# Optimization experiments

Hardware: AMD Instinct MI355X
Metric: run time of the kernel (lower is better)

## Reference

```python
import jax, jax.numpy as jnp
import numpy as np

NUM_RELATION = 7

def setup_inputs() -> dict:
    key = jax.random.key(0)
    ks = jax.random.split(key, 12)
    N, E, D, DO, R, DE = 20000, 640000, 512, 512, NUM_RELATION, 59
    inp = {
        "node_feat": jax.random.normal(ks[0], (N, D), dtype=jnp.float32),
        "edge_weight": jax.random.uniform(ks[1], (E,), dtype=jnp.float32),
        "edge_feat": jax.random.normal(ks[2], (E, DE), dtype=jnp.float32),
        "W_lin": jax.random.normal(ks[3], (DO, R * D), dtype=jnp.float32) * 0.02,
        "b_lin": jax.random.normal(ks[4], (DO,), dtype=jnp.float32) * 0.02,
        "W_self": jax.random.normal(ks[5], (DO, D), dtype=jnp.float32) * 0.02,
        "b_self": jax.random.normal(ks[6], (DO,), dtype=jnp.float32) * 0.02,
        "W_edge": jax.random.normal(ks[7], (DO, DE), dtype=jnp.float32) * 0.02,
        "b_edge": jax.random.normal(ks[8], (DO,), dtype=jnp.float32) * 0.02,
        "node_in": jax.random.randint(ks[9], (E,), 0, N, dtype=jnp.int64) if jax.config.jax_enable_x64 else jax.random.randint(ks[9], (E,), 0, N).astype(jnp.int32),
        "node_out": jax.random.randint(ks[10], (E,), 0, N).astype(jnp.int32),
        "relation": jax.random.randint(ks[11], (E,), 0, R).astype(jnp.int32),
    }
    inp["node_in"] = inp["node_in"].astype(jnp.int32)
    return inp


def reference(node_feat, edge_weight, edge_feat, W_lin, b_lin, W_self, b_self,
              W_edge, b_edge, node_in, node_out, relation):
    N, D = node_feat.shape
    R = NUM_RELATION
    # segment id: node_out * R + relation  (column index in sparse (N, N*R) adjacency)
    seg = node_out * R + relation  # [E]
    # update = adjacency.T @ input  == scatter-add of weighted source features
    msg = node_feat[node_in] * edge_weight[:, None]               # [E, D]
    update = jax.ops.segment_sum(msg, seg, num_segments=N * R)    # [N*R, D]
    # edge_linear path: edge_update scattered with the same segment ids
    edge_msg = (edge_feat @ W_edge.T + b_edge) * edge_weight[:, None]  # [E, D]
    update = update + jax.ops.segment_sum(edge_msg, seg, num_segments=N * R)
    update = update.reshape(N, R * D)                             # [N, R*D]
    # combine: linear(update) + self_loop(input), then relu
    out = update @ W_lin.T + b_lin + node_feat @ W_self.T + b_self
    return jax.nn.relu(out)
```

## Files before the change

kernel.cpp:

```cpp
#include <hip/hip_runtime.h>
#include <stdint.h>

typedef unsigned short u16;
typedef __attribute__((ext_vector_type(8))) __bf16 bf16x8;
typedef __attribute__((ext_vector_type(8))) unsigned short u16x8;
typedef __attribute__((ext_vector_type(4))) float f32x4;

#define NREL 7
#define DIM  512
#define DEDGE 59
#define KC   420
#define KCP  448
#define KU   3584
#define KTOT 4544

__device__ __forceinline__ float bf2f(u16 u) {
  union { unsigned u; float f; } c; c.u = ((unsigned)u) << 16; return c.f;
}
__device__ __forceinline__ u16 f2bf(float f) {
  union { float f; unsigned u; } c; c.f = f;
  unsigned r = ((c.u >> 16) & 1u) + 0x7FFFu;
  return (u16)((c.u + r) >> 16);
}

__device__ __forceinline__ void gload16(const void* g, void* l) {
  __builtin_amdgcn_global_load_lds(
      (__attribute__((address_space(1))) void*)g,
      (__attribute__((address_space(3))) void*)l, 16, 0, 0);
}

__global__ void convA(const float* __restrict__ in, u16* __restrict__ out, int total4) {
  int i = blockIdx.x * 256 + threadIdx.x;
  if (i >= total4) return;
  float4 v = ((const float4*)in)[i];
  ushort4 r;
  r.x = f2bf(v.x); r.y = f2bf(v.y); r.z = f2bf(v.z); r.w = f2bf(v.w);
  ((ushort4*)out)[i] = r;
}

__global__ void buildBW(const float* __restrict__ W_lin, const float* __restrict__ W_self,
                        u16* __restrict__ Bfull, int total4) {
  int gid = blockIdx.x * 256 + threadIdx.x;
  if (gid >= total4) return;
  int idx = gid * 4;
  int o = idx >> 12;
  int k = idx & 4095;
  const float* src = (k < KU) ? (W_lin + (size_t)o * KU + k)
                              : (W_self + (size_t)o * DIM + (k - KU));
  float4 v = *(const float4*)src;
  ushort4 rr;
  rr.x = f2bf(v.x); rr.y = f2bf(v.y); rr.z = f2bf(v.z); rr.w = f2bf(v.w);
  *(ushort4*)(Bfull + (size_t)o * KTOT + k) = rr;
}

__global__ __launch_bounds__(512) void buildCx(const float* __restrict__ W_edge,
                                               const float* __restrict__ b_edge,
                                               const float* __restrict__ W_lin,
                                               u16* __restrict__ Bfull) {
  int c = blockIdx.x;
  int o = threadIdx.x;
  u16* dst = Bfull + (size_t)o * KTOT + KU + DIM;
  if (c >= KC) { dst[c] = 0; return; }
  __shared__ float col[DIM];
  int r;
  if (c < NREL * DEDGE) {
    r = c / DEDGE;
    int de = c - r * DEDGE;
    col[o] = W_edge[(size_t)o * DEDGE + de];
  } else {
    r = c - NREL * DEDGE;
    col[o] = b_edge[o];
  }
  __syncthreads();
  const float* wrow = W_lin + (size_t)o * KU + (size_t)r * DIM;
  float acc = 0.f;
#pragma unroll 8
  for (int d = 0; d < DIM; ++d) acc += col[d] * wrow[d];
  dst[c] = f2bf(acc);
}

__global__ void countK2(const int* __restrict__ node_out, const int* __restrict__ relation,
                        int* __restrict__ counts2, int E) {
  int e = blockIdx.x * 256 + threadIdx.x;
  if (e < E) atomicAdd(&counts2[node_out[e] * 8 + relation[e]], 1);
}

__global__ void baseK(const int* __restrict__ counts2, int* __restrict__ offs2,
                      int* __restrict__ cursor2, int* __restrict__ totalCtr, int N) {
  int n = blockIdx.x * 256 + threadIdx.x;
  if (n >= N) return;
  int cnt[NREL];
  int s = 0;
#pragma unroll
  for (int r = 0; r < NREL; ++r) { cnt[r] = counts2[n * 8 + r]; s += cnt[r]; }
  int base = atomicAdd(totalCtr, s);
#pragma unroll
  for (int r = 0; r < NREL; ++r) {
    offs2[n * 8 + r] = base;
    cursor2[n * 8 + r] = base;
    base += cnt[r];
  }
  offs2[n * 8 + 7] = base;
}

__global__ void fillK2(const int* __restrict__ node_in, const int* __restrict__ node_out,
                       const int* __restrict__ relation, const float* __restrict__ ew,
                       int* __restrict__ cursor2, uint4* __restrict__ quads, int E) {
  int e = blockIdx.x * 256 + threadIdx.x;
  if (e >= E) return;
  int p = atomicAdd(&cursor2[node_out[e] * 8 + relation[e]], 1);
  quads[p] = make_uint4((unsigned)node_in[e], __float_as_uint(ew[e]), (unsigned)e, 0u);
}

__global__ __launch_bounds__(256) void aggK(const u16* __restrict__ NF,
                                            const float* __restrict__ ef,
                                            const uint4* __restrict__ quads,
                                            const int* __restrict__ offs2,
                                            u16* __restrict__ U,
                                            u16* __restrict__ G) {
  int n = blockIdx.x;
  int wid = threadIdx.x >> 6, lane = threadIdx.x & 63;
  int o0 = lane * 8;
  u16* urow = U + (size_t)n * KU;
  u16* grow = G + (size_t)n * KCP;
  if (wid == 3 && lane < KCP - KC) grow[KC + lane] = 0;
  int base = n * 8;
  for (int r = wid; r < NREL; r += 4) {
    int p0 = offs2[base + r], p1 = offs2[base + r + 1];
    float a[8];
#pragma unroll
    for (int j = 0; j < 8; ++j) a[j] = 0.f;
    float ag = 0.f;
    if (p0 < p1) {
      uint4 q = quads[p0];
      for (int p = p0; p < p1; ++p) {
        uint4 qn = (p + 1 < p1) ? quads[p + 1] : q;
        int src = __builtin_amdgcn_readfirstlane((int)q.x);
        float w = __uint_as_float(__builtin_amdgcn_readfirstlane(q.y));
        int e = __builtin_amdgcn_readfirstlane((int)q.z);
        u16x8 hv = *(const u16x8*)(NF + (size_t)src * DIM + o0);
        float vef = (lane < DEDGE) ? ef[(size_t)e * DEDGE + lane] : 1.0f;
#pragma unroll
        for (int j = 0; j < 8; ++j) a[j] += w * bf2f(hv[j]);
        ag += w * vef;
        q = qn;
      }
    }
    u16x8 st;
#pragma unroll
    for (int j = 0; j < 8; ++j) st[j] = f2bf(a[j]);
    *(u16x8*)(urow + (size_t)r * DIM + o0) = st;
    if (lane < DEDGE) grow[r * DEDGE + lane] = f2bf(ag);
    else if (lane == DEDGE) grow[NREL * DEDGE + r] = f2bf(ag);
  }
}

__global__ __launch_bounds__(256) void gemm_br(const u16* __restrict__ U,
                                               const u16* __restrict__ NF,
                                               const u16* __restrict__ G,
                                               const u16* __restrict__ Bt,
                                               const float* __restrict__ b_lin,
                                               const float* __restrict__ b_self,
                                               float* __restrict__ Cout, int M) {
  __shared__ __align__(16) u16 sA[3][128 * 32];
  __shared__ __align__(16) u16 sB[3][128 * 32];
  const int tid = threadIdx.x;
  const int w = tid >> 6, l = tid & 63;
  const int lr = l & 15, kg = l >> 4;
  const int sl = kg ^ ((lr >> 1) & 3);

  const int id = blockIdx.x;
  const int npan = gridDim.x >> 2;
  const int nfull = (npan >> 3) << 3;
  int p, c;
  if (id < nfull * 4) {
    int g = id >> 5, r = id & 31;
    p = g * 8 + (r & 7);
    c = r >> 3;
  } else {
    int t = id - nfull * 4;
    p = nfull + (t >> 2);
    c = t & 3;
  }
  const int m0 = p * 128, n0 = c * 128;
  const int wr = w >> 1, wc = w & 1;
  f32x4 acc[4][4];
  const f32x4 z4 = {0.f, 0.f, 0.f, 0.f};
#pragma unroll
  for (int i = 0; i < 4; ++i)
#pragma unroll
    for (int j = 0; j < 4; ++j) acc[i][j] = z4;

  const int ktiles = KTOT / 32;

  auto stage = [&](int kt, int b) {
    const u16* Ab; int astr, ac0;
    if (kt < 112)      { Ab = U;  astr = KU;  ac0 = kt * 32; }
    else if (kt < 128) { Ab = NF; astr = DIM; ac0 = kt * 32 - KU; }
    else               { Ab = G;  astr = KCP; ac0 = kt * 32 - (KU + DIM); }
    const int k0 = kt * 32;
#pragma unroll
    for (int t = 0; t < 2; ++t) {
      int idx = w * 128 + t * 64 + l;
      int row = idx >> 2, kp = idx & 3;
      int s = kp ^ ((row >> 1) & 3);
      int gm = m0 + row; gm = gm < M ? gm : M - 1;
      gload16(Ab + (size_t)gm * astr + ac0 + s * 8,
              (char*)sA[b] + (size_t)idx * 16);
    }
#pragma unroll
    for (int t = 0; t < 2; ++t) {
      int idx = w * 128 + t * 64 + l;
      int row = idx >> 2, kp = idx & 3;
      int s = kp ^ ((row >> 1) & 3);
      gload16(Bt + (size_t)(n0 + row) * KTOT + k0 + s * 8,
              (char*)sB[b] + (size_t)idx * 16);
    }
  };

  stage(0, 0);
  stage(1, 1);
  asm volatile("s_waitcnt vmcnt(4)" ::: "memory");
  __builtin_amdgcn_s_barrier();
  __builtin_amdgcn_sched_barrier(0);

  for (int kt = 0; kt < ktiles; ++kt) {
    const int cur = kt % 3;
    if (kt + 2 < ktiles) stage(kt + 2, (kt + 2) % 3);
    bf16x8 af[4], bfr[4];
#pragma unroll
    for (int i = 0; i < 4; ++i)
      af[i] = *(const bf16x8*)(sA[cur] + (size_t)(wr * 64 + i * 16 + lr) * 32 + sl * 8);
#pragma unroll
    for (int j = 0; j < 4; ++j)
      bfr[j] = *(const bf16x8*)(sB[cur] + (size_t)(wc * 64 + j * 16 + lr) * 32 + sl * 8);
#pragma unroll
    for (int i = 0; i < 4; ++i)
#pragma unroll
      for (int j = 0; j < 4; ++j)
        acc[i][j] = __builtin_amdgcn_mfma_f32_16x16x32_bf16(af[i], bfr[j], acc[i][j], 0, 0, 0);
    if (kt + 2 < ktiles) {
      asm volatile("s_waitcnt vmcnt(4)" ::: "memory");
    } else {
      asm volatile("s_waitcnt vmcnt(0)" ::: "memory");
    }
    __builtin_amdgcn_s_barrier();
    __builtin_amdgcn_sched_barrier(0);
  }
#pragma unroll
  for (int i = 0; i < 4; ++i) {
#pragma unroll
    for (int j = 0; j < 4; ++j) {
      int gj = n0 + wc * 64 + j * 16 + lr;
      float bias = b_lin[gj] + b_self[gj];
#pragma unroll
      for (int v = 0; v < 4; ++v) {
        int gm = m0 + wr * 64 + i * 16 + kg * 4 + v;
        if (gm < M)
          ((float*)Cout)[(size_t)gm * DIM + gj] = fmaxf(acc[i][j][v] + bias, 0.f);
      }
    }
  }
}

extern "C" void kernel_launch(void* const* d_in, const int* in_sizes, int n_in,
                              void* d_out, int out_size, void* d_ws, size_t ws_size,
                              hipStream_t stream) {
  const float* node_feat = (const float*)d_in[0];
  const float* edge_weight = (const float*)d_in[1];
  const float* edge_feat = (const float*)d_in[2];
  const float* W_lin = (const float*)d_in[3];
  const float* b_lin = (const float*)d_in[4];
  const float* W_self = (const float*)d_in[5];
  const float* b_self = (const float*)d_in[6];
  const float* W_edge = (const float*)d_in[7];
  const float* b_edge = (const float*)d_in[8];
  const int* node_in = (const int*)d_in[9];
  const int* node_out = (const int*)d_in[10];
  const int* relation = (const int*)d_in[11];
  float* out = (float*)d_out;

  const int N = in_sizes[0] / DIM;
  const int E = in_sizes[1];

  char* ws = (char*)d_ws;
  size_t off = 0;
  auto take = [&](size_t b) {
    char* p = ws + off;
    off += (b + 255) & ~(size_t)255;
    return p;
  };
  u16* NF       = (u16*)take((size_t)N * DIM * 2);
  u16* Bfull    = (u16*)take((size_t)DIM * KTOT * 2);
  u16* U        = (u16*)take((size_t)N * KU * 2);
  u16* G        = (u16*)take((size_t)N * KCP * 2);
  int* counts2  = (int*)take((size_t)N * 8 * 4);
  int* offs2    = (int*)take((size_t)N * 8 * 4);
  int* cursor2  = (int*)take((size_t)N * 8 * 4);
  int* totalCtr = (int*)take(256);
  uint4* quads  = (uint4*)take((size_t)E * 16);
  if (off > ws_size) return;

  hipMemsetAsync(counts2, 0, (size_t)N * 8 * 4, stream);
  hipMemsetAsync(totalCtr, 0, 256, stream);

  {
    int total4 = N * DIM / 4;
    convA<<<(total4 + 255) / 256, 256, 0, stream>>>(node_feat, NF, total4);
  }
  {
    int total4 = DIM * 4096 / 4;
    buildBW<<<(total4 + 255) / 256, 256, 0, stream>>>(W_lin, W_self, Bfull, total4);
  }
  buildCx<<<KCP, 512, 0, stream>>>(W_edge, b_edge, W_lin, Bfull);

  countK2<<<(E + 255) / 256, 256, 0, stream>>>(node_out, relation, counts2, E);
  baseK<<<(N + 255) / 256, 256, 0, stream>>>(counts2, offs2, cursor2, totalCtr, N);
  fillK2<<<(E + 255) / 256, 256, 0, stream>>>(node_in, node_out, relation, edge_weight,
                                              cursor2, quads, E);

  aggK<<<N, 256, 0, stream>>>(NF, edge_feat, quads, offs2, U, G);

  {
    int npan = (N + 127) / 128;
    gemm_br<<<npan * 4, 256, 0, stream>>>(U, NF, G, Bfull, b_lin, b_self, out, N);
  }
}
```

Measured before the change: 547.7 us.

## Split aggregation into edge-feature gather and column-partitioned node-feature gather

The single fused aggregation kernel is split into two launches. One handles the edge-feature weighted sums per node. The other uses 8 blocks of 64 threads per node, each covering a 64-column slice. Within a block, 8 edge groups process edges in parallel and are then reduced with cross-lane shuffles. This aims to expose more memory-level parallelism on the irregular gather, instead of one wave walking every edge of a relation serially. The cost is more blocks, repeated reads of the quad list per column slice, and a second launch.

```diff
diff --git a/kernel.cpp b/kernel.cpp
--- a/kernel.cpp
+++ b/kernel.cpp
@@ -112,46 +112,69 @@
   quads[p] = make_uint4((unsigned)node_in[e], __float_as_uint(ew[e]), (unsigned)e, 0u);
 }
 
-__global__ __launch_bounds__(256) void aggK(const u16* __restrict__ NF,
-                                            const float* __restrict__ ef,
-                                            const uint4* __restrict__ quads,
-                                            const int* __restrict__ offs2,
-                                            u16* __restrict__ U,
-                                            u16* __restrict__ G) {
-  int n = blockIdx.x;
-  int wid = threadIdx.x >> 6, lane = threadIdx.x & 63;
-  int o0 = lane * 8;
+__global__ __launch_bounds__(64) void aggP(const u16* __restrict__ NF,
+                                           const uint4* __restrict__ quads,
+                                           const int* __restrict__ offs2,
+                                           u16* __restrict__ U, int N) {
+  int bid = blockIdx.x;
+  int dp = bid / N;
+  int n  = bid - dp * N;
+  int l = threadIdx.x;
+  int grp = l >> 3, gl = l & 7;
+  int c0 = dp * 64 + gl * 8;
+  int base = n * 8;
   u16* urow = U + (size_t)n * KU;
-  u16* grow = G + (size_t)n * KCP;
-  if (wid == 3 && lane < KCP - KC) grow[KC + lane] = 0;
-  int base = n * 8;
-  for (int r = wid; r < NREL; r += 4) {
+  for (int r = 0; r < NREL; ++r) {
     int p0 = offs2[base + r], p1 = offs2[base + r + 1];
     float a[8];
 #pragma unroll
     for (int j = 0; j < 8; ++j) a[j] = 0.f;
-    float ag = 0.f;
-    if (p0 < p1) {
-      uint4 q = quads[p0];
-      for (int p = p0; p < p1; ++p) {
-        uint4 qn = (p + 1 < p1) ? quads[p + 1] : q;
-        int src = __builtin_amdgcn_readfirstlane((int)q.x);
-        float w = __uint_as_float(__builtin_amdgcn_readfirstlane(q.y));
-        int e = __builtin_amdgcn_readfirstlane((int)q.z);
-        u16x8 hv = *(const u16x8*)(NF + (size_t)src * DIM + o0);
-        float vef = (lane < DEDGE) ? ef[(size_t)e * DEDGE + lane] : 1.0f;
-#pragma unroll
-        for (int j = 0; j < 8; ++j) a[j] += w * bf2f(hv[j]);
-        ag += w * vef;
-        q = qn;
-      }
-    }
-    u16x8 st;
-#pragma unroll
-    for (int j = 0; j < 8; ++j) st[j] = f2bf(a[j]);
-    *(u16x8*)(urow + (size_t)r * DIM + o0) = st;
-    if (lane < DEDGE) grow[r * DEDGE + lane] = f2bf(ag);
-    else if (lane == DEDGE) grow[NREL * DEDGE + r] = f2bf(ag);
+    for (int p = p0 + grp; p < p1; p += 8) {
+      uint4 q = quads[p];
+      float w = __uint_as_float(q.y);
+      int src = (int)q.x;
+      u16x8 hv = *(const u16x8*)(NF + (size_t)src * DIM + c0);
+#pragma unroll
+      for (int j = 0; j < 8; ++j) a[j] += w * bf2f(hv[j]);
+    }
+#pragma unroll
+    for (int j = 0; j < 8; ++j) {
+      a[j] += __shfl_xor(a[j], 8);
+      a[j] += __shfl_xor(a[j], 16);
+      a[j] += __shfl_xor(a[j], 32);
+    }
+    if (grp == 0) {
+      u16x8 st;
+#pragma unroll
+      for (int j = 0; j < 8; ++j) st[j] = f2bf(a[j]);
+      *(u16x8*)(urow + (size_t)r * DIM + c0) = st;
+    }
+  }
+}
+
+__global__ __launch_bounds__(64) void gatherG2(const float* __restrict__ ef,
+                                               const uint4* __restrict__ quads,
+                                               const int* __restrict__ offs2,
+                                               u16* __restrict__ G) {
+  int n = blockIdx.x;
+  int lane = threadIdx.x;
+  u16* grow = G + (size_t)n * KCP;
+  int base = n * 8;
+  for (int r = 0; r < NREL; ++r) {
+    int p0 = offs2[base + r], p1 = offs2[base + r + 1];
+    float acc = 0.f;
+    for (int p = p0; p < p1; ++p) {
+      uint4 q = quads[p];
+      int e = __builtin_amdgcn_readfirstlane((int)q.z);
+      float w = __uint_as_float(__builtin_amdgcn_readfirstlane(q.y));
+      float v = (lane < DEDGE) ? ef[(size_t)e * DEDGE + lane] : 1.0f;
+      acc += w * v;
+    }
+    if (lane < DEDGE) grow[r * DEDGE + lane] = f2bf(acc);
+    else if (lane == DEDGE) grow[NREL * DEDGE + r] = f2bf(acc);
+  }
+  if (lane >= 60) {
+    for (int c = KC + (lane - 60); c < KCP; c += 4) grow[c] = 0;
   }
 }
 
@@ -319,7 +342,8 @@
   fillK2<<<(E + 255) / 256, 256, 0, stream>>>(node_in, node_out, relation, edge_weight,
                                               cursor2, quads, E);
 
-  aggK<<<N, 256, 0, stream>>>(NF, edge_feat, quads, offs2, U, G);
+  gatherG2<<<N, 64, 0, stream>>>(edge_feat, quads, offs2, G);
+  aggP<<<8 * N, 64, 0, stream>>>(NF, quads, offs2, U, N);
 
   {
     int npan = (N + 127) / 128;
```

Measured after the change: 643.4 us. +17.5%, slower.

## Split edge-feature and node-feature aggregation into separate block roles; vectorize buildCx

Applied to the files above, without the earlier changes.

The aggregation kernel now launches two kinds of blocks. One kind has each wavefront handle a single node and accumulate the edge-feature sums across all relations. The other kind only gathers node features per relation, so the gather loop no longer also reads edge features. This is meant to cut per-iteration latency and balance the work better. In exchange it drops the quad prefetch and reads the quad list twice. buildCx also switches to float4 loads of W_lin.

```diff
diff --git a/kernel.cpp b/kernel.cpp
--- a/kernel.cpp
+++ b/kernel.cpp
@@ -72,10 +72,14 @@
     col[o] = b_edge[o];
   }
   __syncthreads();
-  const float* wrow = W_lin + (size_t)o * KU + (size_t)r * DIM;
+  const float4* wv = (const float4*)(W_lin + (size_t)o * KU + (size_t)r * DIM);
   float acc = 0.f;
-#pragma unroll 8
-  for (int d = 0; d < DIM; ++d) acc += col[d] * wrow[d];
+#pragma unroll 4
+  for (int d4 = 0; d4 < DIM / 4; ++d4) {
+    float4 wq = wv[d4];
+    acc += col[d4 * 4 + 0] * wq.x + col[d4 * 4 + 1] * wq.y
+         + col[d4 * 4 + 2] * wq.z + col[d4 * 4 + 3] * wq.w;
+  }
   dst[c] = f2bf(acc);
 }
 
@@ -112,46 +116,59 @@
   quads[p] = make_uint4((unsigned)node_in[e], __float_as_uint(ew[e]), (unsigned)e, 0u);
 }
 
-__global__ __launch_bounds__(256) void aggK(const u16* __restrict__ NF,
-                                            const float* __restrict__ ef,
-                                            const uint4* __restrict__ quads,
-                                            const int* __restrict__ offs2,
-                                            u16* __restrict__ U,
-                                            u16* __restrict__ G) {
-  int n = blockIdx.x;
+__global__ __launch_bounds__(256) void aggBoth(const u16* __restrict__ NF,
+                                               const float* __restrict__ ef,
+                                               const uint4* __restrict__ quads,
+                                               const int* __restrict__ offs2,
+                                               u16* __restrict__ U,
+                                               u16* __restrict__ G,
+                                               int N, int ngg) {
+  int bid = blockIdx.x;
   int wid = threadIdx.x >> 6, lane = threadIdx.x & 63;
-  int o0 = lane * 8;
-  u16* urow = U + (size_t)n * KU;
-  u16* grow = G + (size_t)n * KCP;
-  if (wid == 3 && lane < KCP - KC) grow[KC + lane] = 0;
-  int base = n * 8;
-  for (int r = wid; r < NREL; r += 4) {
-    int p0 = offs2[base + r], p1 = offs2[base + r + 1];
-    float a[8];
-#pragma unroll
-    for (int j = 0; j < 8; ++j) a[j] = 0.f;
-    float ag = 0.f;
-    if (p0 < p1) {
-      uint4 q = quads[p0];
+  if (bid < ngg) {
+    int n = bid * 4 + wid;
+    if (n >= N) return;
+    u16* grow = G + (size_t)n * KCP;
+    int base = n * 8;
+    for (int r = 0; r < NREL; ++r) {
+      int p0 = offs2[base + r], p1 = offs2[base + r + 1];
+      float acc = 0.f;
       for (int p = p0; p < p1; ++p) {
-        uint4 qn = (p + 1 < p1) ? quads[p + 1] : q;
+        uint4 q = quads[p];
+        int e = __builtin_amdgcn_readfirstlane((int)q.z);
+        float w = __uint_as_float(__builtin_amdgcn_readfirstlane(q.y));
+        float v = (lane < DEDGE) ? ef[(size_t)e * DEDGE + lane] : 1.0f;
+        acc += w * v;
+      }
+      if (lane < DEDGE) grow[r * DEDGE + lane] = f2bf(acc);
+      else if (lane == DEDGE) grow[NREL * DEDGE + r] = f2bf(acc);
+    }
+    if (lane >= 60) {
+      for (int c = KC + (lane - 60); c < KCP; c += 4) grow[c] = 0;
+    }
+  } else {
+    int n = bid - ngg;
+    int o0 = lane * 8;
+    u16* urow = U + (size_t)n * KU;
+    int base = n * 8;
+    for (int r = wid; r < NREL; r += 4) {
+      int p0 = offs2[base + r], p1 = offs2[base + r + 1];
+      float a[8];
+#pragma unroll
+      for (int j = 0; j < 8; ++j) a[j] = 0.f;
+      for (int p = p0; p < p1; ++p) {
+        uint4 q = quads[p];
         int src = __builtin_amdgcn_readfirstlane((int)q.x);
         float w = __uint_as_float(__builtin_amdgcn_readfirstlane(q.y));
-        int e = __builtin_amdgcn_readfirstlane((int)q.z);
         u16x8 hv = *(const u16x8*)(NF + (size_t)src * DIM + o0);
-        float vef = (lane < DEDGE) ? ef[(size_t)e * DEDGE + lane] : 1.0f;
 #pragma unroll
         for (int j = 0; j < 8; ++j) a[j] += w * bf2f(hv[j]);
-        ag += w * vef;
-        q = qn;
       }
-    }
-    u16x8 st;
-#pragma unroll
-    for (int j = 0; j < 8; ++j) st[j] = f2bf(a[j]);
-    *(u16x8*)(urow + (size_t)r * DIM + o0) = st;
-    if (lane < DEDGE) grow[r * DEDGE + lane] = f2bf(ag);
-    else if (lane == DEDGE) grow[NREL * DEDGE + r] = f2bf(ag);
+      u16x8 st;
+#pragma unroll
+      for (int j = 0; j < 8; ++j) st[j] = f2bf(a[j]);
+      *(u16x8*)(urow + (size_t)r * DIM + o0) = st;
+    }
   }
 }
 
@@ -319,7 +336,10 @@
   fillK2<<<(E + 255) / 256, 256, 0, stream>>>(node_in, node_out, relation, edge_weight,
                                               cursor2, quads, E);
 
-  aggK<<<N, 256, 0, stream>>>(NF, edge_feat, quads, offs2, U, G);
+  {
+    int ngg = (N + 3) / 4;
+    aggBoth<<<ngg + N, 256, 0, stream>>>(NF, edge_feat, quads, offs2, U, G, N, ngg);
+  }
 
   {
     int npan = (N + 127) / 128;
```

Measured after the change: 502.6 us. -8.2%, faster.
